# Kernel tuning notes

Measured on AMD Instinct MI355X. Metric: run time of the kernel, lower is better.

## Reference

```python
import jax, jax.numpy as jnp
import numpy as np

D_MODEL, NUM_HEADS, D_FF = 1024, 16, 4096
HEAD_DIM = D_MODEL // NUM_HEADS
EPS = 1e-5


def _layernorm(x, g, b):
    m = jnp.mean(x, axis=-1, keepdims=True)
    v = jnp.mean((x - m) ** 2, axis=-1, keepdims=True)
    return (x - m) * jax.lax.rsqrt(v + EPS) * g + b


def setup_inputs() -> dict:
    key = jax.random.key(0)
    ks = jax.random.split(key, 16)
    N, S = 4, 2048
    x = jax.random.normal(ks[0], (N, S, D_MODEL), dtype=jnp.float32)
    # mask broadcastable against energy of shape (N, S, H, H) -- see notes: code
    # computes per-position head-vs-head attention, not SxS attention.
    mask = jax.random.randint(ks[1], (N, 1, 1, NUM_HEADS), 0, 2, dtype=jnp.int32)
    s = 0.02
    return {
        "x": x,
        "Wqkv": jax.random.normal(ks[2], (D_MODEL, 3 * D_MODEL), dtype=jnp.float32) * s,
        "bqkv": jnp.zeros((3 * D_MODEL,), jnp.float32),
        "Wo": jax.random.normal(ks[3], (D_MODEL, D_MODEL), dtype=jnp.float32) * s,
        "bo": jnp.zeros((D_MODEL,), jnp.float32),
        "g1": jnp.ones((D_MODEL,), jnp.float32),
        "beta1": jnp.zeros((D_MODEL,), jnp.float32),
        "W1": jax.random.normal(ks[4], (D_MODEL, D_FF), dtype=jnp.float32) * s,
        "bf1": jnp.zeros((D_FF,), jnp.float32),
        "W2": jax.random.normal(ks[5], (D_FF, D_MODEL), dtype=jnp.float32) * s,
        "bf2": jnpp if False else jnp.zeros((D_MODEL,), jnp.float32),
        "g2": jnp.ones((D_MODEL,), jnp.float32),
        "beta2": jnp.zeros((D_MODEL,), jnp.float32),
        "mask": mask,
    }


def reference(x, Wqkv, bqkv, Wo, bo, g1, beta1, W1, bf1, W2, bf2, g2, beta2, mask):
    N, S, D = x.shape
    H, hd = NUM_HEADS, HEAD_DIM
    # fused QKV projection
    qkv = (x @ Wqkv + bqkv).reshape(N, S, 3, H, hd).transpose(2, 0, 3, 1, 4)
    q, k, v = qkv[0], qkv[1], qkv[2]  # each (N, H, S, hd)
    # faithful to torch einsum 'nqhd,nkhd->nhqk' on (N,H,S,hd) operands:
    # energy[n,s,i,j] = sum_d q[n,i,s,d] * k[n,j,s,d]  -> (N, S, H, H)
    energy = jnp.einsum('nise,njse->nsij', q, k)
    energy = jnp.where(mask == 0, jnp.float32(-1e20), energy)
    attn = jax.nn.softmax(energy / np.sqrt(hd).astype(np.float32), axis=3)
    # torch einsum 'nhql,nlhd->nqhd': out[n,i,s,d] = sum_l attn[n,s,i,l]*v[n,l,s,d]
    out = jnp.einsum('nsil,nlse->nise', attn, v)  # (N, H, S, hd)
    out = out.reshape(N, S, D)  # row-major flatten, exactly as torch .reshape
    attn_out = out @ Wo + bo
    h = _layernorm(attn_out + x, g1, beta1)
    ff = jax.nn.relu(h @ W1 + bf1) @ W2 + bf2  # dropout = identity (eval)
    return _layernorm(ff + h, g2, beta2)
```

## Files before the change

### kernel.cpp

```cpp
#include <hip/hip_runtime.h>
#include <cstdint>
#include <cstddef>


using f32x4  = __attribute__((ext_vector_type(4))) float;
using bf16x8 = __attribute__((ext_vector_type(8))) __bf16;

__device__ __forceinline__ unsigned short f2b(float f) {
  union { float f; uint32_t u; } v; v.f = f;
  uint32_t r = v.u + 0x7FFFu + ((v.u >> 16) & 1u);
  return (unsigned short)(r >> 16);
}
__device__ __forceinline__ float b2f(unsigned short u) {
  union { uint32_t u; float f; } v; v.u = ((uint32_t)u) << 16;
  return v.f;
}

__device__ __forceinline__ void gload_lds16(const unsigned short* g,
                                            unsigned short* l) {
  __builtin_amdgcn_global_load_lds(
      (const __attribute__((address_space(1))) unsigned int*)g,
      (__attribute__((address_space(3))) unsigned int*)l, 16, 0, 0);
}

__device__ __forceinline__ void barrier_sync() {
  __builtin_amdgcn_sched_barrier(0);
  __builtin_amdgcn_s_barrier();
  __builtin_amdgcn_sched_barrier(0);
}
template <int N>
__device__ __forceinline__ void vmwait() {
  __builtin_amdgcn_sched_barrier(0);
  if constexpr (N == 0) asm volatile("s_waitcnt vmcnt(0)");
  if constexpr (N == 6) asm volatile("s_waitcnt vmcnt(6)");
  __builtin_amdgcn_sched_barrier(0);
}

__global__ __launch_bounds__(256) void prep_kernel(
    const float* __restrict__ Wqkv, unsigned short* __restrict__ WqkvT,
    const float* __restrict__ Wo,   unsigned short* __restrict__ WoT,
    const float* __restrict__ W1,   unsigned short* __restrict__ W1T,
    const float* __restrict__ W2,   unsigned short* __restrict__ W2T,
    const float* __restrict__ x,    unsigned short* __restrict__ xb) {
  __shared__ float tile[32][33];
  const int b = blockIdx.x, tid = threadIdx.x;
  if (b >= 12288) {
    for (int i = (b - 12288) * 256 + tid; i < 2097152; i += 2048 * 256) {
      float4 v = ((const float4*)x)[i];
      uint32_t lo = (uint32_t)f2b(v.x) | ((uint32_t)f2b(v.y) << 16);
      uint32_t hi = (uint32_t)f2b(v.z) | ((uint32_t)f2b(v.w) << 16);
      ((uint2*)xb)[i] = make_uint2(lo, hi);
    }
    return;
  }
  const float* W; unsigned short* WT; int K, N, jb, kb;
  if (b < 3072)       { W=Wqkv; WT=WqkvT; K=1024; N=3072; jb=b%96;          kb=b/96; }
  else if (b < 4096)  { W=Wo;   WT=WoT;   K=1024; N=1024; jb=(b-3072)%32;   kb=(b-3072)/32; }
  else if (b < 8192)  { W=W1;   WT=W1T;   K=1024; N=4096; jb=(b-4096)%128;  kb=(b-4096)/128; }
  else                { W=W2;   WT=W2T;   K=4096; N=1024; jb=(b-8192)%32;   kb=(b-8192)/32; }
  const int j0 = jb * 32, k0 = kb * 32;
  const int tx = tid & 31, ty = tid >> 5;
#pragma unroll
  for (int i = 0; i < 4; ++i)
    tile[ty + 8 * i][tx] = W[(size_t)(k0 + ty + 8 * i) * N + j0 + tx];
  __syncthreads();
#pragma unroll
  for (int i = 0; i < 4; ++i)
    WT[(size_t)(j0 + ty + 8 * i) * K + k0 + tx] = f2b(tile[tx][ty + 8 * i]);
}

template <bool SPLITK, bool OUTB, bool RELU>
__global__ __launch_bounds__(512, 2) void gemm8_kernel(
    const unsigned short* __restrict__ A, const unsigned short* __restrict__ B,
    const float* __restrict__ bias, void* __restrict__ C,
    unsigned short* __restrict__ Cp1, unsigned short* __restrict__ Cp2,
    int M, int N, int Ks, int Kd, int nbn) {
  constexpr int HT = 128 * 64;
  __shared__ unsigned short lds[8 * HT];

  const int tid  = threadIdx.x;
  const int lane = tid & 63, wave = tid >> 6;
  const int wm = wave >> 2, wn = wave & 3;
  const int lr = lane & 15, lk = lane >> 4;
  const int x7 = lr & 7;

  const int nwg = gridDim.x, cpx = nwg >> 3, id = blockIdx.x;
  const int wg = (id & 7) * cpx + (id >> 3);
  int bm, bn, sk;
  if (SPLITK) { bm = wg >> 3; bn = (wg & 7) >> 1; sk = wg & 1; }
  else        { bm = wg / nbn; bn = wg % nbn; sk = 0; }

  const unsigned short* Ab = A + (size_t)bm * 256 * Ks + (size_t)sk * Kd;
  const unsigned short* Bb = B + (size_t)bn * 256 * Ks + (size_t)sk * Kd;

  const int srow = tid >> 3;
  const int scol = ((tid & 7) ^ (srow & 7)) * 8;
  const int ldst = wave * 8 * 64;

  const int NT = Kd >> 6;

  f32x4 acc[8][4] = {};
  bf16x8 aC[4][2], bC[2][2], bH[2][2];

#define SLOT_A(B_, H_) (((B_)*4 + (H_)) * HT)
#define SLOT_B(B_, H_) (((B_)*4 + 2 + (H_)) * HT)
#define STG_A(B_, H_, T_)                                                     \
  _Pragma("unroll") for (int i_ = 0; i_ < 2; ++i_)                            \
      gload_lds16(Ab + (size_t)((H_)*128 + i_ * 64 + srow) * Ks + (T_)*64 + scol, \
                  &lds[SLOT_A(B_, H_) + i_ * 64 * 64 + ldst])
#define STG_B(B_, H_, T_)                                                     \
  _Pragma("unroll") for (int i_ = 0; i_ < 2; ++i_)                            \
      gload_lds16(Bb + (size_t)((H_)*128 + i_ * 64 + srow) * Ks + (T_)*64 + scol, \
                  &lds[SLOT_B(B_, H_) + i_ * 64 * 64 + ldst])
#define RD_A(DST, B_, H_)                                                     \
  _Pragma("unroll") for (int mi_ = 0; mi_ < 4; ++mi_)                         \
    _Pragma("unroll") for (int kk_ = 0; kk_ < 2; ++kk_)                       \
      DST[mi_][kk_] = *(const bf16x8*)&lds[SLOT_A(B_, H_) +                   \
          (wm * 64 + mi_ * 16 + lr) * 64 + ((kk_ * 4 + lk) ^ x7) * 8]
#define RD_B(DST, B_, H_)                                                     \
  _Pragma("unroll") for (int ni_ = 0; ni_ < 2; ++ni_)                         \
    _Pragma("unroll") for (int kk_ = 0; kk_ < 2; ++kk_)                       \
      DST[ni_][kk_] = *(const bf16x8*)&lds[SLOT_B(B_, H_) +                   \
          (wn * 32 + ni_ * 16 + lr) * 64 + ((kk_ * 4 + lk) ^ x7) * 8]
#define MM(AS, BS, MH, NH)                                                    \
  do {                                                                        \
    __builtin_amdgcn_s_setprio(1);                                            \
    _Pragma("unroll") for (int mi_ = 0; mi_ < 4; ++mi_)                       \
      _Pragma("unroll") for (int ni_ = 0; ni_ < 2; ++ni_)                     \
        _Pragma("unroll") for (int kk_ = 0; kk_ < 2; ++kk_)                   \
          acc[(MH)*4 + mi_][(NH)*2 + ni_] =                                   \
              __builtin_amdgcn_mfma_f32_16x16x32_bf16(                        \
                  AS[mi_][kk_], BS[ni_][kk_],                                 \
                  acc[(MH)*4 + mi_][(NH)*2 + ni_], 0, 0, 0);                  \
    __builtin_amdgcn_s_setprio(0);                                            \
  } while (0)

  STG_A(0, 0, 0); STG_B(0, 0, 0); STG_B(0, 1, 0); STG_A(0, 1, 0);
  STG_A(1, 0, 1); STG_B(1, 1, 1); STG_A(1, 1, 1);
  vmwait<0>();
  barrier_sync();

  for (int t = 0; t < NT; t += 2) {
    const bool st = (t + 2 < NT);
    RD_A(aC, 0, 0); RD_B(bH, 0, 0);
    STG_B(1, 0, t + 1);
    barrier_sync(); MM(aC, bH, 0, 0); barrier_sync();
    RD_B(bC, 0, 1);
    if (st) STG_A(0, 0, t + 2);
    barrier_sync(); MM(aC, bC, 0, 1); barrier_sync();
    RD_A(aC, 0, 1);
    if (st) STG_B(0, 1, t + 2);
    barrier_sync(); MM(aC, bC, 1, 1); barrier_sync();
    if (st) { STG_A(0, 1, t + 2); vmwait<6>(); } else { vmwait<0>(); }
    barrier_sync(); MM(aC, bH, 1, 0); barrier_sync();
    RD_A(aC, 1, 0); RD_B(bH, 1, 0);
    if (st) STG_B(0, 0, t + 2);
    barrier_sync(); MM(aC, bH, 0, 0); barrier_sync();
    RD_B(bC, 1, 1);
    if (st) STG_A(1, 0, t + 3);
    barrier_sync(); MM(aC, bC, 0, 1); barrier_sync();
    RD_A(aC, 1, 1);
    if (st) STG_B(1, 1, t + 3);
    barrier_sync(); MM(aC, bC, 1, 1); barrier_sync();
    if (st) { STG_A(1, 1, t + 3); vmwait<6>(); }
    barrier_sync(); MM(aC, bH, 1, 0); barrier_sync();
  }

#undef MM
#undef RD_A
#undef RD_B
#undef STG_A
#undef STG_B
#undef SLOT_A
#undef SLOT_B

  const int orow0 = bm * 256 + wm * 64;
  const int ocol0 = bn * 256 + wn * 32;
#pragma unroll
  for (int mh = 0; mh < 2; ++mh)
#pragma unroll
    for (int nh = 0; nh < 2; ++nh)
#pragma unroll
      for (int ni = 0; ni < 2; ++ni) {
        int col = ocol0 + nh * 128 + ni * 16 + lr;
        float bv = bias[col];
#pragma unroll
        for (int mi = 0; mi < 4; ++mi)
#pragma unroll
          for (int r = 0; r < 4; ++r) {
            int row = orow0 + mh * 128 + mi * 16 + lk * 4 + r;
            float val = acc[mh * 4 + mi][nh * 2 + ni][r];
            if (SPLITK) {
              unsigned short* dst = sk ? Cp2 : Cp1;
              dst[(size_t)row * N + col] = f2b(sk ? val : val + bv);
            } else {
              val += bv;
              if (RELU) val = fmaxf(val, 0.f);
              if (OUTB)
                ((unsigned short*)C)[(size_t)row * N + col] = f2b(val);
              else
                ((float*)C)[(size_t)row * N + col] = val;
            }
          }
      }
}

__global__ __launch_bounds__(256) void attn_kernel(
    const unsigned short* __restrict__ qkv, const int* __restrict__ mask,
    unsigned short* __restrict__ outb) {
  __shared__ float sq[16][68], sk[16][68], sv[16][68];
  __shared__ float sp[16][17];
  const int pos = blockIdx.x;
  const int n = pos >> 11, s = pos & 2047;
  const int tid = threadIdx.x;
  const unsigned short* row = qkv + (size_t)pos * 3072;
#pragma unroll
  for (int it = 0; it < 3; ++it) {
    uint2 raw = *(const uint2*)(row + it * 1024 + tid * 4);
    float f0 = b2f((unsigned short)(raw.x & 0xffffu));
    float f1 = b2f((unsigned short)(raw.x >> 16));
    float f2 = b2f((unsigned short)(raw.y & 0xffffu));
    float f3 = b2f((unsigned short)(raw.y >> 16));
    float(*dst)[68] = (it == 0) ? sq : (it == 1) ? sk : sv;
    int r = tid >> 4, d = (tid & 15) * 4;
    dst[r][d] = f0; dst[r][d + 1] = f1; dst[r][d + 2] = f2; dst[r][d + 3] = f3;
  }
  __syncthreads();
  {
    const int i = tid >> 4, j = tid & 15;
    float e = 0.f;
#pragma unroll
    for (int d = 0; d < 64; d += 4) {
      float4 qa = *(const float4*)&sq[i][d];
      float4 kb = *(const float4*)&sk[j][d];
      e += qa.x * kb.x + qa.y * kb.y + qa.z * kb.z + qa.w * kb.w;
    }
    if (mask[n * 16 + j] == 0) e = -1e20f;
    e *= 0.125f;
    float mx = e;
#pragma unroll
    for (int o = 8; o > 0; o >>= 1) mx = fmaxf(mx, __shfl_xor(mx, o, 16));
    float pe = __expf(e - mx);
    float sm = pe;
#pragma unroll
    for (int o = 8; o > 0; o >>= 1) sm += __shfl_xor(sm, o, 16);
    sp[i][j] = pe / sm;
  }
  __syncthreads();
  {
    const int w = tid >> 6, d = tid & 63;
    float o0 = 0, o1 = 0, o2 = 0, o3 = 0;
#pragma unroll
    for (int l = 0; l < 16; ++l) {
      float vv = sv[l][d];
      o0 += sp[w][l] * vv;      o1 += sp[w + 4][l] * vv;
      o2 += sp[w + 8][l] * vv;  o3 += sp[w + 12][l] * vv;
    }
    outb[(((size_t)n * 16 + w     ) * 2048 + s) * 64 + d] = f2b(o0);
    outb[(((size_t)n * 16 + w + 4 ) * 2048 + s) * 64 + d] = f2b(o1);
    outb[(((size_t)n * 16 + w + 8 ) * 2048 + s) * 64 + d] = f2b(o2);
    outb[(((size_t)n * 16 + w + 12) * 2048 + s) * 64 + d] = f2b(o3);
  }
}

template <bool RB16>
__global__ __launch_bounds__(256) void ln_kernel(
    const unsigned short* __restrict__ P1, const unsigned short* __restrict__ P2,
    const void* __restrict__ R,
    const float* __restrict__ g, const float* __restrict__ be,
    float* __restrict__ outf, unsigned short* __restrict__ outb) {
  const int row = blockIdx.x, tid = threadIdx.x;
  const size_t base = (size_t)row * 1024 + tid * 4;
  uint2 p = *(const uint2*)(P1 + base);
  uint2 q = *(const uint2*)(P2 + base);
  float x0 = b2f((unsigned short)(p.x & 0xffffu)) + b2f((unsigned short)(q.x & 0xffffu));
  float x1 = b2f((unsigned short)(p.x >> 16))     + b2f((unsigned short)(q.x >> 16));
  float x2 = b2f((unsigned short)(p.y & 0xffffu)) + b2f((unsigned short)(q.y & 0xffffu));
  float x3 = b2f((unsigned short)(p.y >> 16))     + b2f((unsigned short)(q.y >> 16));
  if (RB16) {
    uint2 r = *(const uint2*)((const unsigned short*)R + base);
    x0 += b2f((unsigned short)(r.x & 0xffffu));
    x1 += b2f((unsigned short)(r.x >> 16));
    x2 += b2f((unsigned short)(r.y & 0xffffu));
    x3 += b2f((unsigned short)(r.y >> 16));
  } else {
    float4 r = *(const float4*)((const float*)R + base);
    x0 += r.x; x1 += r.y; x2 += r.z; x3 += r.w;
  }
  float s = x0 + x1 + x2 + x3;
#pragma unroll
  for (int o = 32; o > 0; o >>= 1) s += __shfl_xor(s, o);
  __shared__ float red[4];
  const int lane = tid & 63, wv = tid >> 6;
  if (lane == 0) red[wv] = s;
  __syncthreads();
  float mean = (red[0] + red[1] + red[2] + red[3]) * (1.f / 1024.f);
  float d0 = x0 - mean, d1 = x1 - mean, d2 = x2 - mean, d3 = x3 - mean;
  float qd = d0 * d0 + d1 * d1 + d2 * d2 + d3 * d3;
#pragma unroll
  for (int o = 32; o > 0; o >>= 1) qd += __shfl_xor(qd, o);
  __syncthreads();
  if (lane == 0) red[wv] = qd;
  __syncthreads();
  float var = (red[0] + red[1] + red[2] + red[3]) * (1.f / 1024.f);
  float rs = rsqrtf(var + 1e-5f);
  const int col = tid * 4;
  float4 gv = *(const float4*)(g + col);
  float4 bv = *(const float4*)(be + col);
  float y0 = d0 * rs * gv.x + bv.x;
  float y1 = d1 * rs * gv.y + bv.y;
  float y2 = d2 * rs * gv.z + bv.z;
  float y3 = d3 * rs * gv.w + bv.w;
  if (outf) *(float4*)(outf + base) = make_float4(y0, y1, y2, y3);
  if (outb) {
    uint32_t lo = (uint32_t)f2b(y0) | ((uint32_t)f2b(y1) << 16);
    uint32_t hi = (uint32_t)f2b(y2) | ((uint32_t)f2b(y3) << 16);
    *(uint2*)(outb + base) = make_uint2(lo, hi);
  }
}

extern "C" void kernel_launch(void* const* d_in, const int* in_sizes, int n_in,
                              void* d_out, int out_size, void* d_ws,
                              size_t ws_size, hipStream_t stream) {
  (void)in_sizes; (void)n_in; (void)out_size; (void)ws_size;
  const float* x     = (const float*)d_in[0];
  const float* Wqkv  = (const float*)d_in[1];
  const float* bqkv  = (const float*)d_in[2];
  const float* Wo    = (const float*)d_in[3];
  const float* bo    = (const float*)d_in[4];
  const float* g1    = (const float*)d_in[5];
  const float* beta1 = (const float*)d_in[6];
  const float* W1    = (const float*)d_in[7];
  const float* bf1   = (const float*)d_in[8];
  const float* W2    = (const float*)d_in[9];
  const float* bf2   = (const float*)d_in[10];
  const float* g2    = (const float*)d_in[11];
  const float* beta2 = (const float*)d_in[12];
  const int*   mask  = (const int*)d_in[13];
  float* out = (float*)d_out;

  char* ws = (char*)d_ws;
  unsigned short* WqkvT = (unsigned short*)(ws + 0);
  unsigned short* WoT   = (unsigned short*)(ws + 6291456);
  unsigned short* W1T   = (unsigned short*)(ws + 8388608);
  unsigned short* W2T   = (unsigned short*)(ws + 16777216);
  unsigned short* xb    = (unsigned short*)(ws + 25165824);
  unsigned short* h_b   = (unsigned short*)(ws + 41943040);
  unsigned short* aop1  = (unsigned short*)(ws + 58720256);
  unsigned short* aop2  = (unsigned short*)(ws + 75497472);
  unsigned short* qkvb  = (unsigned short*)(ws + 92274688);
  unsigned short* aob   = (unsigned short*)(ws + 142606336);
  unsigned short* ff1   = qkvb;
  unsigned short* ffp1  = aop1;
  unsigned short* ffp2  = aop2;

  prep_kernel<<<14336, 256, 0, stream>>>(Wqkv, WqkvT, Wo, WoT, W1, W1T, W2, W2T, x, xb);

  gemm8_kernel<false, true, false><<<dim3(384), 512, 0, stream>>>(
      xb, WqkvT, bqkv, qkvb, nullptr, nullptr, 8192, 3072, 1024, 1024, 12);
  attn_kernel<<<8192, 256, 0, stream>>>(qkvb, mask, aob);
  gemm8_kernel<true, false, false><<<dim3(256), 512, 0, stream>>>(
      aob, WoT, bo, nullptr, aop1, aop2, 8192, 1024, 1024, 512, 4);
  ln_kernel<false><<<8192, 256, 0, stream>>>(aop1, aop2, x, g1, beta1, nullptr, h_b);
  gemm8_kernel<false, true, true><<<dim3(512), 512, 0, stream>>>(
      h_b, W1T, bf1, ff1, nullptr, nullptr, 8192, 4096, 1024, 1024, 16);
  gemm8_kernel<true, false, false><<<dim3(256), 512, 0, stream>>>(
      ff1, W2T, bf2, nullptr, ffp1, ffp2, 8192, 1024, 4096, 2048, 4);
  ln_kernel<true><<<8192, 256, 0, stream>>>(ffp1, ffp2, h_b, g2, beta2, out, nullptr);
}
```

Measured before the change: 296.8 us.

## Restructure GEMM main loop into two-phase pipeline with fewer barriers

```diff
diff --git a/kernel.cpp b/kernel.cpp
--- a/kernel.cpp
+++ b/kernel.cpp
@@ -32,7 +32,7 @@
 __device__ __forceinline__ void vmwait() {
   __builtin_amdgcn_sched_barrier(0);
   if constexpr (N == 0) asm volatile("s_waitcnt vmcnt(0)");
-  if constexpr (N == 6) asm volatile("s_waitcnt vmcnt(6)");
+  if constexpr (N == 4) asm volatile("s_waitcnt vmcnt(4)");
   __builtin_amdgcn_sched_barrier(0);
 }
 
@@ -70,7 +70,7 @@
 }
 
 template <bool SPLITK, bool OUTB, bool RELU>
-__global__ __launch_bounds__(512, 2) void gemm8_kernel(
+__global__ __launch_bounds__(512, 2) void gemm2p_kernel(
     const unsigned short* __restrict__ A, const unsigned short* __restrict__ B,
     const float* __restrict__ bias, void* __restrict__ C,
     unsigned short* __restrict__ Cp1, unsigned short* __restrict__ Cp2,
@@ -100,7 +100,7 @@
   const int NT = Kd >> 6;
 
   f32x4 acc[8][4] = {};
-  bf16x8 aC[4][2], bC[2][2], bH[2][2];
+  bf16x8 aC[4][2], bH[2][2], bC[2][2];
 
 #define SLOT_A(B_, H_) (((B_)*4 + (H_)) * HT)
 #define SLOT_B(B_, H_) (((B_)*4 + 2 + (H_)) * HT)
@@ -112,63 +112,59 @@
   _Pragma("unroll") for (int i_ = 0; i_ < 2; ++i_)                            \
       gload_lds16(Bb + (size_t)((H_)*128 + i_ * 64 + srow) * Ks + (T_)*64 + scol, \
                   &lds[SLOT_B(B_, H_) + i_ * 64 * 64 + ldst])
-#define RD_A(DST, B_, H_)                                                     \
+#define RDA_K(DST, B_, H_, KK)                                                \
   _Pragma("unroll") for (int mi_ = 0; mi_ < 4; ++mi_)                         \
-    _Pragma("unroll") for (int kk_ = 0; kk_ < 2; ++kk_)                       \
-      DST[mi_][kk_] = *(const bf16x8*)&lds[SLOT_A(B_, H_) +                   \
-          (wm * 64 + mi_ * 16 + lr) * 64 + ((kk_ * 4 + lk) ^ x7) * 8]
-#define RD_B(DST, B_, H_)                                                     \
+      DST[mi_][KK] = *(const bf16x8*)&lds[SLOT_A(B_, H_) +                    \
+          (wm * 64 + mi_ * 16 + lr) * 64 + (((KK)*4 + lk) ^ x7) * 8]
+#define RDB_K(DST, B_, H_, KK)                                                \
   _Pragma("unroll") for (int ni_ = 0; ni_ < 2; ++ni_)                         \
-    _Pragma("unroll") for (int kk_ = 0; kk_ < 2; ++kk_)                       \
-      DST[ni_][kk_] = *(const bf16x8*)&lds[SLOT_B(B_, H_) +                   \
-          (wn * 32 + ni_ * 16 + lr) * 64 + ((kk_ * 4 + lk) ^ x7) * 8]
-#define MM(AS, BS, MH, NH)                                                    \
-  do {                                                                        \
-    __builtin_amdgcn_s_setprio(1);                                            \
-    _Pragma("unroll") for (int mi_ = 0; mi_ < 4; ++mi_)                       \
-      _Pragma("unroll") for (int ni_ = 0; ni_ < 2; ++ni_)                     \
-        _Pragma("unroll") for (int kk_ = 0; kk_ < 2; ++kk_)                   \
-          acc[(MH)*4 + mi_][(NH)*2 + ni_] =                                   \
-              __builtin_amdgcn_mfma_f32_16x16x32_bf16(                        \
-                  AS[mi_][kk_], BS[ni_][kk_],                                 \
-                  acc[(MH)*4 + mi_][(NH)*2 + ni_], 0, 0, 0);                  \
-    __builtin_amdgcn_s_setprio(0);                                            \
-  } while (0)
+      DST[ni_][KK] = *(const bf16x8*)&lds[SLOT_B(B_, H_) +                    \
+          (wn * 32 + ni_ * 16 + lr) * 64 + (((KK)*4 + lk) ^ x7) * 8]
+#define MM8(AS, BS, MH, NH, KK)                                               \
+  _Pragma("unroll") for (int mi_ = 0; mi_ < 4; ++mi_)                         \
+    _Pragma("unroll") for (int ni_ = 0; ni_ < 2; ++ni_)                       \
+      acc[(MH)*4 + mi_][(NH)*2 + ni_] =                                       \
+          __builtin_amdgcn_mfma_f32_16x16x32_bf16(                            \
+              AS[mi_][KK], BS[ni_][KK], acc[(MH)*4 + mi_][(NH)*2 + ni_], 0, 0, 0)
+#define SB0() __builtin_amdgcn_sched_barrier(0)
 
   STG_A(0, 0, 0); STG_B(0, 0, 0); STG_B(0, 1, 0); STG_A(0, 1, 0);
-  STG_A(1, 0, 1); STG_B(1, 1, 1); STG_A(1, 1, 1);
-  vmwait<0>();
+  STG_A(1, 0, 1); STG_B(1, 0, 1);
+  vmwait<4>();
   barrier_sync();
 
-  for (int t = 0; t < NT; t += 2) {
-    const bool st = (t + 2 < NT);
-    RD_A(aC, 0, 0); RD_B(bH, 0, 0);
-    STG_B(1, 0, t + 1);
-    barrier_sync(); MM(aC, bH, 0, 0); barrier_sync();
-    RD_B(bC, 0, 1);
-    if (st) STG_A(0, 0, t + 2);
-    barrier_sync(); MM(aC, bC, 0, 1); barrier_sync();
-    RD_A(aC, 0, 1);
-    if (st) STG_B(0, 1, t + 2);
-    barrier_sync(); MM(aC, bC, 1, 1); barrier_sync();
-    if (st) { STG_A(0, 1, t + 2); vmwait<6>(); } else { vmwait<0>(); }
-    barrier_sync(); MM(aC, bH, 1, 0); barrier_sync();
-    RD_A(aC, 1, 0); RD_B(bH, 1, 0);
-    if (st) STG_B(0, 0, t + 2);
-    barrier_sync(); MM(aC, bH, 0, 0); barrier_sync();
-    RD_B(bC, 1, 1);
-    if (st) STG_A(1, 0, t + 3);
-    barrier_sync(); MM(aC, bC, 0, 1); barrier_sync();
-    RD_A(aC, 1, 1);
-    if (st) STG_B(1, 1, t + 3);
-    barrier_sync(); MM(aC, bC, 1, 1); barrier_sync();
-    if (st) { STG_A(1, 1, t + 3); vmwait<6>(); }
-    barrier_sync(); MM(aC, bH, 1, 0); barrier_sync();
-  }
-
-#undef MM
-#undef RD_A
-#undef RD_B
+  for (int t = 0; t < NT; ++t) {
+    const int p = t & 1;
+    const bool s1 = (t + 1 < NT), s2 = (t + 2 < NT);
+    if (s1) { STG_A(p ^ 1, 1, t + 1); STG_B(p ^ 1, 1, t + 1); }
+    RDA_K(aC, p, 0, 0); RDB_K(bH, p, 0, 0);
+    RDA_K(aC, p, 0, 1); RDB_K(bH, p, 0, 1);
+    RDB_K(bC, p, 1, 0); RDB_K(bC, p, 1, 1);
+    barrier_sync();
+    __builtin_amdgcn_s_setprio(1);
+    MM8(aC, bH, 0, 0, 0); SB0();
+    MM8(aC, bH, 0, 0, 1); SB0();
+    MM8(aC, bC, 0, 1, 0); SB0();
+    MM8(aC, bC, 0, 1, 1);
+    __builtin_amdgcn_s_setprio(0);
+    barrier_sync();
+    if (s2) { STG_A(p, 0, t + 2); STG_B(p, 0, t + 2); }
+    RDA_K(aC, p, 1, 0); RDA_K(aC, p, 1, 1);
+    if (s2) vmwait<4>(); else if (s1) vmwait<0>();
+    barrier_sync();
+    __builtin_amdgcn_s_setprio(1);
+    MM8(aC, bC, 1, 1, 0); SB0();
+    MM8(aC, bH, 1, 0, 0); SB0();
+    MM8(aC, bC, 1, 1, 1); SB0();
+    MM8(aC, bH, 1, 0, 1);
+    __builtin_amdgcn_s_setprio(0);
+    barrier_sync();
+  }
+
+#undef SB0
+#undef MM8
+#undef RDA_K
+#undef RDB_K
 #undef STG_A
 #undef STG_B
 #undef SLOT_A
@@ -356,15 +352,15 @@
 
   prep_kernel<<<14336, 256, 0, stream>>>(Wqkv, WqkvT, Wo, WoT, W1, W1T, W2, W2T, x, xb);
 
-  gemm8_kernel<false, true, false><<<dim3(384), 512, 0, stream>>>(
+  gemm2p_kernel<false, true, false><<<dim3(384), 512, 0, stream>>>(
       xb, WqkvT, bqkv, qkvb, nullptr, nullptr, 8192, 3072, 1024, 1024, 12);
   attn_kernel<<<8192, 256, 0, stream>>>(qkvb, mask, aob);
-  gemm8_kernel<true, false, false><<<dim3(256), 512, 0, stream>>>(
+  gemm2p_kernel<true, false, false><<<dim3(256), 512, 0, stream>>>(
       aob, WoT, bo, nullptr, aop1, aop2, 8192, 1024, 1024, 512, 4);
   ln_kernel<false><<<8192, 256, 0, stream>>>(aop1, aop2, x, g1, beta1, nullptr, h_b);
-  gemm8_kernel<false, true, true><<<dim3(512), 512, 0, stream>>>(
+  gemm2p_kernel<false, true, true><<<dim3(512), 512, 0, stream>>>(
       h_b, W1T, bf1, ff1, nullptr, nullptr, 8192, 4096, 1024, 1024, 16);
-  gemm8_kernel<true, false, false><<<dim3(256), 512, 0, stream>>>(
+  gemm2p_kernel<true, false, false><<<dim3(256), 512, 0, stream>>>(
       ff1, W2T, bf2, nullptr, ffp1, ffp2, 8192, 1024, 4096, 2048, 4);
   ln_kernel<true><<<8192, 256, 0, stream>>>(ffp1, ffp2, h_b, g2, beta2, out, nullptr);
 }
```

After: 299.6 us. Within noise of the previous version (+0.9%).
